# Kernel tuning notes

Measured on AMD Instinct MI355X. Metric: run time of the kernel, lower is better.

Reference implementation:

```python
import jax, jax.numpy as jnp
import numpy as np

WS = 8       # window size
HEADS = 2    # num_heads hardcoded in CFPT's Swin_transformer blocks


def _to_windows(t, ws):
    # t: [B, H, W, C] -> [B*nWin, ws*ws, C]
    B, H, W, C = t.shape
    t = t.reshape(B, H // ws, ws, W // ws, ws, C)
    t = t.transpose(0, 1, 3, 2, 4, 5)
    return t.reshape(-1, ws * ws, C)


def _from_windows(t, B, H, W, ws):
    # t: [B*nWin, ws*ws, C] -> [B, H, W, C]
    C = t.shape[-1]
    t = t.reshape(B, H // ws, W // ws, ws, ws, C)
    t = t.transpose(0, 1, 3, 2, 4, 5)
    return t.reshape(B, H, W, C)


def swin_cross_attn(x, y, Wq, Wk, Wv, Wo):
    # Windowed cross-attention: queries from x, keys/values from y.
    # x, y: [B, C, H, W]; Wq/Wk/Wv/Wo: [C, C] (bias-free, no position embedding).
    B, C, H, W = x.shape
    dh = C // HEADS
    xw = _to_windows(x.transpose(0, 2, 3, 1), WS)   # [Bn, T, C], T = WS*WS
    yw = _to_windows(y.transpose(0, 2, 3, 1), WS)
    q = jnp.einsum('btc,dc->btd', xw, Wq)
    k = jnp.einsum('btc,dc->btd', yw, Wk)
    v = jnp.einsum('btc,dc->btd', yw, Wv)
    Bn, T, _ = q.shape
    q = q.reshape(Bn, T, HEADS, dh)
    k = k.reshape(Bn, T, HEADS, dh)
    v = v.reshape(Bn, T, HEADS, dh)
    scale = jnp.asarray(dh, x.dtype) ** -0.5
    scores = jnp.einsum('bqhd,bkhd->bhqk', q, k) * scale   # [Bn, H, T, T]
    attn = jax.nn.softmax(scores, axis=-1)
    o = jnp.einsum('bhqk,bkhd->bqhd', attn, v).reshape(Bn, T, C)
    o = jnp.einsum('btc,dc->btd', o, Wo)
    return _from_windows(o, B, H, W, WS).transpose(0, 3, 1, 2)  # [B, C, H, W]


def setup_inputs() -> dict:
    key = jax.random.key(0)
    ks = jax.random.split(key, 6)
    C = 256
    shapes = [(4, C, 128, 128), (4, C, 64, 64), (4, C, 32, 32), (4, C, 16, 16)]
    feats = [jax.random.normal(ks[i], s, jnp.float32) for i, s in enumerate(shapes)]
    w1 = jax.random.normal(ks[4], (4, 4, C, C), jnp.float32) * 0.02
    w2 = jax.random.normal(ks[5], (4, 4, C, C), jnp.float32) * 0.02
    return {"feat0": feats[0], "feat1": feats[1], "feat2": feats[2],
            "feat3": feats[3], "w1": w1, "w2": w2}


def reference(feat0, feat1, feat2, feat3, w1, w2):
    feats = [feat0, feat1, feat2, feat3]
    l = feats[0].shape[0] // 2
    outs = []
    for i, f in enumerate(feats):
        f1, f2 = f[:l], f[l:]
        # sequential cross-update, as in the original loop body
        f1 = jax.nn.relu(f1 + swin_cross_attn(f1, f2, w1[i, 0], w1[i, 1], w1[i, 2], w1[i, 3]))
        f2 = jax.nn.relu(f2 + swin_cross_attn(f2, f1, w2[i, 0], w2[i, 1], w2[i, 2], w2[i, 3]))
        outs.append(jnp.concatenate([f1, f2], axis=0))
    return tuple(outs)
```

## Files before the change

### kernel.cpp

```cpp
#include <hip/hip_runtime.h>


using bf16x8 = __attribute__((ext_vector_type(8))) __bf16;
using f32x4  = __attribute__((ext_vector_type(4))) float;
using u16x4  = __attribute__((ext_vector_type(4))) unsigned short;
using u16x8  = __attribute__((ext_vector_type(8))) unsigned short;

__device__ __forceinline__ unsigned short f2bf(float f){
  unsigned int x = __float_as_uint(f);
  x += 0x7FFFu + ((x >> 16) & 1u);
  return (unsigned short)(x >> 16);
}
__device__ __forceinline__ float bf2f(unsigned short u){
  return __uint_as_float((unsigned int)u << 16);
}
__device__ __forceinline__ void store_bf4(unsigned short* dst, f32x4 v){
  u16x4 o;
  o[0]=f2bf(v[0]); o[1]=f2bf(v[1]); o[2]=f2bf(v[2]); o[3]=f2bf(v[3]);
  *reinterpret_cast<u16x4*>(dst) = o;
}

#define MFMA16 __builtin_amdgcn_mfma_f32_16x16x32_bf16

__global__ void wcvt_kernel(const float* __restrict__ w1,
                            const float* __restrict__ w2,
                            unsigned short* __restrict__ dst){
  int i = blockIdx.x * 256 + threadIdx.x;
  const float4* src = (i < 262144) ? (reinterpret_cast<const float4*>(w1) + i)
                                   : (reinterpret_cast<const float4*>(w2) + (i - 262144));
  float4 v = *src;
  u16x4 o; o[0]=f2bf(v.x); o[1]=f2bf(v.y); o[2]=f2bf(v.z); o[3]=f2bf(v.w);
  reinterpret_cast<u16x4*>(dst)[i] = o;
}

__global__ __launch_bounds__(256, 2) void xpose_kernel(
    const float* __restrict__ g0, const float* __restrict__ g1,
    const float* __restrict__ g2, const float* __restrict__ g3,
    unsigned short* __restrict__ Ft)
{
  __shared__ float T[64][65];
  int bid = blockIdx.x;
  int r; const float* feat; int Hl; size_t tbase;
  if (bid < 4096){ r = bid;        feat = g0; Hl = 128; tbase = 0; }
  else if (bid < 5120){ r = bid - 4096; feat = g1; Hl = 64;  tbase = 65536; }
  else if (bid < 5376){ r = bid - 5120; feat = g2; Hl = 32;  tbase = 81920; }
  else { r = bid - 5376; feat = g3; Hl = 16;  tbase = 86016; }
  size_t HW = (size_t)Hl * Hl;
  int hw64 = (int)(HW >> 6);
  int bat = r / (4 * hw64);
  int r2 = r - bat * 4 * hw64;
  int ct = r2 / hw64, hwt = r2 - ct * hw64;

  const float* src = feat + (size_t)bat * HW * 256 + (size_t)(ct * 64) * HW + (size_t)hwt * 64;
  int tid = threadIdx.x;
  int cq = tid >> 4, hw0 = (tid & 15) * 4;
  #pragma unroll
  for (int p = 0; p < 4; ++p){
    int c = p * 16 + cq;
    const float* sp = src + (size_t)c * HW + hw0;
    float4 v = *reinterpret_cast<const float4*>(sp);
    T[c][hw0] = v.x; T[c][hw0+1] = v.y; T[c][hw0+2] = v.z; T[c][hw0+3] = v.w;
  }
  __syncthreads();
  unsigned short* dst = Ft + (tbase + (size_t)bat * HW + (size_t)hwt * 64) * 256 + ct * 64;
  #pragma unroll
  for (int p = 0; p < 2; ++p){
    int id = p * 256 + tid;
    int t = id >> 3, c0 = (id & 7) * 8;
    u16x8 o;
    #pragma unroll
    for (int j = 0; j < 8; ++j) o[j] = f2bf(T[c0 + j][t]);
    *reinterpret_cast<u16x8*>(dst + (size_t)t * 256 + c0) = o;
  }
}

__global__ __launch_bounds__(256, 2) void untrans_kernel(
    const unsigned short* __restrict__ Gt, float* __restrict__ outb)
{
  __shared__ float T[64][65];
  int bid = blockIdx.x;
  int r; int Hl; size_t tbase, ooff;
  if (bid < 4096){ r = bid;        Hl = 128; tbase = 0;     ooff = 0; }
  else if (bid < 5120){ r = bid - 4096; Hl = 64; tbase = 65536; ooff = 16777216; }
  else if (bid < 5376){ r = bid - 5120; Hl = 32; tbase = 81920; ooff = 20971520; }
  else { r = bid - 5376; Hl = 16; tbase = 86016; ooff = 22020096; }
  size_t HW = (size_t)Hl * Hl;
  int hw64 = (int)(HW >> 6);
  int bat = r / (4 * hw64);
  int r2 = r - bat * 4 * hw64;
  int ct = r2 / hw64, hwt = r2 - ct * hw64;

  const unsigned short* src = Gt + (tbase + (size_t)bat * HW + (size_t)hwt * 64) * 256 + ct * 64;
  int tid = threadIdx.x;
  #pragma unroll
  for (int p = 0; p < 2; ++p){
    int id = p * 256 + tid;
    int t = id >> 3, c0 = (id & 7) * 8;
    u16x8 v = *reinterpret_cast<const u16x8*>(src + (size_t)t * 256 + c0);
    #pragma unroll
    for (int j = 0; j < 8; ++j) T[t][c0 + j] = bf2f(v[j]);
  }
  __syncthreads();
  float* dst = outb + ooff + (size_t)bat * HW * 256 + (size_t)(ct * 64) * HW + (size_t)hwt * 64;
  int cq = tid >> 4, hw0 = (tid & 15) * 4;
  #pragma unroll
  for (int p = 0; p < 4; ++p){
    int c = p * 16 + cq;
    float4 v;
    v.x = T[hw0][c]; v.y = T[hw0+1][c]; v.z = T[hw0+2][c]; v.w = T[hw0+3][c];
    *reinterpret_cast<float4*>(dst + (size_t)c * HW + hw0) = v;
  }
}

struct WinGeo { int H, W, b, lvl; size_t HW, winoff, tbase, ooff; };

__device__ __forceinline__ WinGeo decode_win(int win){
  WinGeo g; int wloc;
  if (win < 512){ g.lvl = 0; wloc = win;      g.H = 128; g.tbase = 0;     g.ooff = 0; }
  else if (win < 640){ g.lvl = 1; wloc = win - 512; g.H = 64; g.tbase = 65536; g.ooff = 16777216; }
  else if (win < 672){ g.lvl = 2; wloc = win - 640; g.H = 32; g.tbase = 81920; g.ooff = 20971520; }
  else { g.lvl = 3; wloc = win - 672; g.H = 16; g.tbase = 86016; g.ooff = 22020096; }
  g.W = g.H; g.HW = (size_t)g.H * g.W;
  int nww = g.H >> 3, npb = nww * nww;
  g.b = wloc / npb;
  int r = wloc - g.b * npb;
  int wh = r / nww, ww = r - wh * nww;
  g.winoff = (size_t)(wh * 8) * g.W + (size_t)(ww * 8);
  return g;
}

__global__ __launch_bounds__(256, 2) void swin_win(
    const unsigned short* __restrict__ Ft, const unsigned short* __restrict__ Gtin,
    const unsigned short* __restrict__ wball,
    unsigned short* __restrict__ Gt, int phase)
{
  __shared__ alignas(16) unsigned short A[64*264];
  __shared__ alignas(16) unsigned short B[256*72];
  int win = blockIdx.x;
  WinGeo g = decode_win(win);
  int tid = threadIdx.x;
  int w = tid >> 6, l = tid & 63, l15 = l & 15, l4 = l >> 4, wd = w * 64;
  int h = w >> 1, tc = w & 1;

  int batx = (phase == 0) ? g.b : g.b + 2;
  const unsigned short* Sx = Ft + (g.tbase + (size_t)batx * g.HW) * 256;
  const unsigned short* Sy = (phase == 0)
      ? Ft + (g.tbase + (size_t)(g.b + 2) * g.HW) * 256
      : Gtin + (g.tbase + (size_t)g.b * g.HW) * 256;
  unsigned short* Gout = Gt + (g.tbase + (size_t)batx * g.HW) * 256;

  size_t rowo[4];
  #pragma unroll
  for (int ni = 0; ni < 4; ++ni){
    int t = ni * 16 + l15;
    rowo[ni] = ((size_t)g.winoff + (size_t)(t >> 3) * g.W + (t & 7)) * 256;
  }
  const unsigned short* Wbase = wball + ((size_t)(phase * 16 + g.lvl * 4) << 16);
  const unsigned short* Wq = Wbase;
  const unsigned short* Wk = Wbase + 65536;
  const unsigned short* Wv = Wbase + 131072;
  const unsigned short* Wo = Wbase + 196608;

  f32x4 av[4][4];
  {
    f32x4 ak[4][4];
    #pragma unroll
    for (int i = 0; i < 4; ++i)
      #pragma unroll
      for (int j = 0; j < 4; ++j){ ak[i][j] = f32x4{0.f,0.f,0.f,0.f}; av[i][j] = f32x4{0.f,0.f,0.f,0.f}; }
    #pragma unroll
    for (int ks = 0; ks < 8; ++ks){
      int k0 = ks * 32 + l4 * 8;
      bf16x8 tf[4], kf[4], vf[4];
      #pragma unroll
      for (int i = 0; i < 4; ++i){
        tf[i] = *reinterpret_cast<const bf16x8*>(Sy + rowo[i] + k0);
        kf[i] = *reinterpret_cast<const bf16x8*>(Wk + (size_t)((wd + i*16 + l15) * 256 + k0));
        vf[i] = *reinterpret_cast<const bf16x8*>(Wv + (size_t)((wd + i*16 + l15) * 256 + k0));
      }
      __builtin_amdgcn_s_setprio(1);
      #pragma unroll
      for (int mi = 0; mi < 4; ++mi)
        #pragma unroll
        for (int ni = 0; ni < 4; ++ni){
          ak[mi][ni] = MFMA16(kf[mi], tf[ni], ak[mi][ni], 0, 0, 0);
          av[mi][ni] = MFMA16(tf[mi], vf[ni], av[mi][ni], 0, 0, 0);
        }
      __builtin_amdgcn_s_setprio(0);
    }
    #pragma unroll
    for (int mi = 0; mi < 4; ++mi){
      int d0 = wd + mi*16 + l4*4;
      #pragma unroll
      for (int ni = 0; ni < 4; ++ni)
        store_bf4(&A[(ni*16 + l15) * 264 + d0], ak[mi][ni]);
    }
  }

  {
    f32x4 aq[4][4];
    #pragma unroll
    for (int i = 0; i < 4; ++i)
      #pragma unroll
      for (int j = 0; j < 4; ++j) aq[i][j] = f32x4{0.f,0.f,0.f,0.f};
    #pragma unroll
    for (int ks = 0; ks < 8; ++ks){
      int k0 = ks * 32 + l4 * 8;
      bf16x8 tf[4], wf[4];
      #pragma unroll
      for (int i = 0; i < 4; ++i){
        tf[i] = *reinterpret_cast<const bf16x8*>(Sx + rowo[i] + k0);
        wf[i] = *reinterpret_cast<const bf16x8*>(Wq + (size_t)((wd + i*16 + l15) * 256 + k0));
      }
      __builtin_amdgcn_s_setprio(1);
      #pragma unroll
      for (int mi = 0; mi < 4; ++mi)
        #pragma unroll
        for (int ni = 0; ni < 4; ++ni)
          aq[mi][ni] = MFMA16(wf[mi], tf[ni], aq[mi][ni], 0, 0, 0);
      __builtin_amdgcn_s_setprio(0);
    }
    #pragma unroll
    for (int mi = 0; mi < 4; ++mi){
      int d0 = wd + mi*16 + l4*4;
      #pragma unroll
      for (int ni = 0; ni < 4; ++ni)
        store_bf4(&B[(ni*16 + l15) * 264 + d0], aq[mi][ni]);
    }
  }
  __syncthreads();

  f32x4 s[4][2];
  #pragma unroll
  for (int i = 0; i < 4; ++i){ s[i][0] = f32x4{0.f,0.f,0.f,0.f}; s[i][1] = f32x4{0.f,0.f,0.f,0.f}; }
  #pragma unroll
  for (int ks = 0; ks < 4; ++ks){
    int k0 = h * 128 + ks * 32 + l4 * 8;
    bf16x8 a[4], bb[2];
    #pragma unroll
    for (int mi = 0; mi < 4; ++mi)
      a[mi] = *reinterpret_cast<const bf16x8*>(&A[(mi*16 + l15) * 264 + k0]);
    #pragma unroll
    for (int ni = 0; ni < 2; ++ni)
      bb[ni] = *reinterpret_cast<const bf16x8*>(&B[(tc*32 + ni*16 + l15) * 264 + k0]);
    __builtin_amdgcn_s_setprio(1);
    #pragma unroll
    for (int mi = 0; mi < 4; ++mi)
      #pragma unroll
      for (int ni = 0; ni < 2; ++ni)
        s[mi][ni] = MFMA16(a[mi], bb[ni], s[mi][ni], 0, 0, 0);
    __builtin_amdgcn_s_setprio(0);
  }
  __syncthreads();

  #pragma unroll
  for (int mi = 0; mi < 4; ++mi){
    int u0 = mi*16 + l4*4;
    #pragma unroll
    for (int ni = 0; ni < 4; ++ni)
      store_bf4(&B[(wd + ni*16 + l15) * 72 + u0], av[mi][ni]);
  }

  const float SCL = 0.08838834764831845f;
  #pragma unroll
  for (int ni = 0; ni < 2; ++ni){
    float m = s[0][ni][0];
    #pragma unroll
    for (int mi = 0; mi < 4; ++mi)
      #pragma unroll
      for (int reg = 0; reg < 4; ++reg) m = fmaxf(m, s[mi][ni][reg]);
    m = fmaxf(m, __shfl_xor(m, 16));
    m = fmaxf(m, __shfl_xor(m, 32));
    float sum = 0.f;
    #pragma unroll
    for (int mi = 0; mi < 4; ++mi)
      #pragma unroll
      for (int reg = 0; reg < 4; ++reg){
        float e = __expf((s[mi][ni][reg] - m) * SCL);
        s[mi][ni][reg] = e; sum += e;
      }
    sum += __shfl_xor(sum, 16);
    sum += __shfl_xor(sum, 32);
    float rs = 1.0f / sum;
    int t = tc*32 + ni*16 + l15;
    #pragma unroll
    for (int mi = 0; mi < 4; ++mi){
      f32x4 pv;
      #pragma unroll
      for (int reg = 0; reg < 4; ++reg) pv[reg] = s[mi][ni][reg] * rs;
      store_bf4(&A[h * 4608 + t * 72 + mi*16 + l4*4], pv);
    }
  }
  __syncthreads();

  f32x4 acc[4][4];
  #pragma unroll
  for (int i = 0; i < 4; ++i)
    #pragma unroll
    for (int j = 0; j < 4; ++j) acc[i][j] = f32x4{0.f,0.f,0.f,0.f};
  #pragma unroll
  for (int ks = 0; ks < 2; ++ks){
    int k0 = ks * 32 + l4 * 8;
    bf16x8 a[4], bb[4];
    #pragma unroll
    for (int mi = 0; mi < 4; ++mi)
      a[mi] = *reinterpret_cast<const bf16x8*>(&B[(wd + mi*16 + l15) * 72 + k0]);
    #pragma unroll
    for (int ni = 0; ni < 4; ++ni)
      bb[ni] = *reinterpret_cast<const bf16x8*>(&A[h * 4608 + (ni*16 + l15) * 72 + k0]);
    __builtin_amdgcn_s_setprio(1);
    #pragma unroll
    for (int mi = 0; mi < 4; ++mi)
      #pragma unroll
      for (int ni = 0; ni < 4; ++ni)
        acc[mi][ni] = MFMA16(a[mi], bb[ni], acc[mi][ni], 0, 0, 0);
    __builtin_amdgcn_s_setprio(0);
  }
  __syncthreads();
  #pragma unroll
  for (int mi = 0; mi < 4; ++mi){
    int c0 = wd + mi*16 + l4*4;
    #pragma unroll
    for (int ni = 0; ni < 4; ++ni)
      store_bf4(&A[(ni*16 + l15) * 264 + c0], acc[mi][ni]);
  }
  __syncthreads();

  #pragma unroll
  for (int i = 0; i < 4; ++i)
    #pragma unroll
    for (int j = 0; j < 4; ++j) acc[i][j] = f32x4{0.f,0.f,0.f,0.f};
  #pragma unroll
  for (int ks = 0; ks < 8; ++ks){
    int k0 = ks * 32 + l4 * 8;
    bf16x8 a[4], bb[4];
    #pragma unroll
    for (int mi = 0; mi < 4; ++mi)
      a[mi] = *reinterpret_cast<const bf16x8*>(Wo + (size_t)((wd + mi*16 + l15) * 256 + k0));
    #pragma unroll
    for (int ni = 0; ni < 4; ++ni)
      bb[ni] = *reinterpret_cast<const bf16x8*>(&A[(ni*16 + l15) * 264 + k0]);
    __builtin_amdgcn_s_setprio(1);
    #pragma unroll
    for (int mi = 0; mi < 4; ++mi)
      #pragma unroll
      for (int ni = 0; ni < 4; ++ni)
        acc[mi][ni] = MFMA16(a[mi], bb[ni], acc[mi][ni], 0, 0, 0);
    __builtin_amdgcn_s_setprio(0);
  }
  __syncthreads();
  #pragma unroll
  for (int mi = 0; mi < 4; ++mi){
    int c0 = wd + mi*16 + l4*4;
    #pragma unroll
    for (int ni = 0; ni < 4; ++ni)
      store_bf4(&A[(ni*16 + l15) * 264 + c0], acc[mi][ni]);
  }
  __syncthreads();

  #pragma unroll
  for (int p = 0; p < 8; ++p){
    int id = p * 256 + tid;
    int t = id >> 5, c = (id & 31) * 8;
    size_t ro = ((size_t)g.winoff + (size_t)(t >> 3) * g.W + (t & 7)) * 256 + c;
    u16x8 ov = *reinterpret_cast<const u16x8*>(&A[t * 264 + c]);
    u16x8 rv = *reinterpret_cast<const u16x8*>(Sx + ro);
    u16x8 o;
    #pragma unroll
    for (int j = 0; j < 8; ++j)
      o[j] = f2bf(fmaxf(bf2f(ov[j]) + bf2f(rv[j]), 0.f));
    *reinterpret_cast<u16x8*>(Gout + ro) = o;
  }
}

__global__ __launch_bounds__(256, 1) void swin_phase(
    const float* __restrict__ g0, const float* __restrict__ g1,
    const float* __restrict__ g2, const float* __restrict__ g3,
    const unsigned short* __restrict__ wball,
    float* __restrict__ outb, int phase)
{
  __shared__ alignas(16) unsigned short R0[64*264];
  __shared__ alignas(16) unsigned short R1[64*264];
  __shared__ alignas(16) unsigned short R2[256*72];
  __shared__ alignas(16) unsigned short R3[64*264];

  int bid = blockIdx.x;
  WinGeo g = decode_win(bid);
  const float* feat = (g.lvl == 0) ? g0 : (g.lvl == 1) ? g1 : (g.lvl == 2) ? g2 : g3;
  size_t CHW = g.HW * 256;

  const float* xsrc; const float* ysrc; float* outp;
  if (phase == 0){
    xsrc = feat + (size_t)g.b * CHW + g.winoff;
    ysrc = feat + (size_t)(g.b + 2) * CHW + g.winoff;
    outp = outb + g.ooff + (size_t)g.b * CHW + g.winoff;
  } else {
    xsrc = feat + (size_t)(g.b + 2) * CHW + g.winoff;
    ysrc = outb + g.ooff + (size_t)g.b * CHW + g.winoff;
    outp = outb + g.ooff + (size_t)(g.b + 2) * CHW + g.winoff;
  }
  const unsigned short* Wq = wball + ((size_t)(phase * 16 + g.lvl * 4) << 16);
  const unsigned short* Wk = Wq + 65536;
  const unsigned short* Wv = Wq + 2 * 65536;
  const unsigned short* Wo = Wq + 3 * 65536;

  int tid = threadIdx.x;
  int w = tid >> 6, l = tid & 63, l15 = l & 15, l4 = l >> 4, wd = w * 64;
  int hi0 = l >> 3, wi0 = l & 7;

  {
    const float* p0 = ysrc + (size_t)hi0 * g.W + wi0;
    #pragma unroll
    for (int oc = 0; oc < 8; ++oc){
      int c0 = (oc * 4 + w) * 8;
      const float* p = p0 + (size_t)c0 * g.HW;
      u16x8 uv;
      #pragma unroll
      for (int j = 0; j < 8; ++j) uv[j] = f2bf(p[(size_t)j * g.HW]);
      *reinterpret_cast<u16x8*>(&R0[l * 264 + c0]) = uv;
    }
  }
  __syncthreads();
  {
    f32x4 acc[4][4];
    #pragma unroll
    for (int i = 0; i < 4; ++i)
      #pragma unroll
      for (int j = 0; j < 4; ++j) acc[i][j] = f32x4{0.f,0.f,0.f,0.f};
    #pragma unroll
    for (int ks = 0; ks < 8; ++ks){
      int k0 = ks * 32 + l4 * 8;
      bf16x8 a[4], bb[4];
      #pragma unroll
      for (int mi = 0; mi < 4; ++mi)
        a[mi] = *reinterpret_cast<const bf16x8*>(Wk + (size_t)((wd + mi*16 + l15) * 256 + k0));
      #pragma unroll
      for (int ni = 0; ni < 4; ++ni)
        bb[ni] = *reinterpret_cast<const bf16x8*>(&R0[(ni*16 + l15) * 264 + k0]);
      #pragma unroll
      for (int mi = 0; mi < 4; ++mi)
        #pragma unroll
        for (int ni = 0; ni < 4; ++ni)
          acc[mi][ni] = MFMA16(a[mi], bb[ni], acc[mi][ni], 0, 0, 0);
    }
    #pragma unroll
    for (int mi = 0; mi < 4; ++mi){
      int d0 = wd + mi*16 + l4*4;
      #pragma unroll
      for (int ni = 0; ni < 4; ++ni)
        store_bf4(&R1[(ni*16 + l15) * 264 + d0], acc[mi][ni]);
    }
  }
  {
    f32x4 acc[4][4];
    #pragma unroll
    for (int i = 0; i < 4; ++i)
      #pragma unroll
      for (int j = 0; j < 4; ++j) acc[i][j] = f32x4{0.f,0.f,0.f,0.f};
    #pragma unroll
    for (int ks = 0; ks < 8; ++ks){
      int k0 = ks * 32 + l4 * 8;
      bf16x8 a[4], bb[4];
      #pragma unroll
      for (int mi = 0; mi < 4; ++mi)
        a[mi] = *reinterpret_cast<const bf16x8*>(&R0[(mi*16 + l15) * 264 + k0]);
      #pragma unroll
      for (int ni = 0; ni < 4; ++ni)
        bb[ni] = *reinterpret_cast<const bf16x8*>(Wv + (size_t)((wd + ni*16 + l15) * 256 + k0));
      #pragma unroll
      for (int mi = 0; mi < 4; ++mi)
        #pragma unroll
        for (int ni = 0; ni < 4; ++ni)
          acc[mi][ni] = MFMA16(a[mi], bb[ni], acc[mi][ni], 0, 0, 0);
    }
    #pragma unroll
    for (int mi = 0; mi < 4; ++mi){
      int u0 = mi*16 + l4*4;
      #pragma unroll
      for (int ni = 0; ni < 4; ++ni)
        store_bf4(&R2[(wd + ni*16 + l15) * 72 + u0], acc[mi][ni]);
    }
  }
  __syncthreads();
  {
    const float* p0 = xsrc + (size_t)hi0 * g.W + wi0;
    #pragma unroll
    for (int oc = 0; oc < 8; ++oc){
      int c0 = (oc * 4 + w) * 8;
      const float* p = p0 + (size_t)c0 * g.HW;
      u16x8 uv;
      #pragma unroll
      for (int j = 0; j < 8; ++j) uv[j] = f2bf(p[(size_t)j * g.HW]);
      *reinterpret_cast<u16x8*>(&R0[l * 264 + c0]) = uv;
    }
  }
  __syncthreads();
  {
    f32x4 acc[4][4];
    #pragma unroll
    for (int i = 0; i < 4; ++i)
      #pragma unroll
      for (int j = 0; j < 4; ++j) acc[i][j] = f32x4{0.f,0.f,0.f,0.f};
    #pragma unroll
    for (int ks = 0; ks < 8; ++ks){
      int k0 = ks * 32 + l4 * 8;
      bf16x8 a[4], bb[4];
      #pragma unroll
      for (int mi = 0; mi < 4; ++mi)
        a[mi] = *reinterpret_cast<const bf16x8*>(Wq + (size_t)((wd + mi*16 + l15) * 256 + k0));
      #pragma unroll
      for (int ni = 0; ni < 4; ++ni)
        bb[ni] = *reinterpret_cast<const bf16x8*>(&R0[(ni*16 + l15) * 264 + k0]);
      #pragma unroll
      for (int mi = 0; mi < 4; ++mi)
        #pragma unroll
        for (int ni = 0; ni < 4; ++ni)
          acc[mi][ni] = MFMA16(a[mi], bb[ni], acc[mi][ni], 0, 0, 0);
    }
    #pragma unroll
    for (int mi = 0; mi < 4; ++mi){
      int d0 = wd + mi*16 + l4*4;
      #pragma unroll
      for (int ni = 0; ni < 4; ++ni)
        store_bf4(&R3[(ni*16 + l15) * 264 + d0], acc[mi][ni]);
    }
  }
  __syncthreads();

  int h = w >> 1, tc = w & 1;
  {
    f32x4 s[4][2];
    #pragma unroll
    for (int i = 0; i < 4; ++i){ s[i][0] = f32x4{0.f,0.f,0.f,0.f}; s[i][1] = f32x4{0.f,0.f,0.f,0.f}; }
    #pragma unroll
    for (int ks = 0; ks < 4; ++ks){
      int k0 = h * 128 + ks * 32 + l4 * 8;
      bf16x8 a[4], bb[2];
      #pragma unroll
      for (int mi = 0; mi < 4; ++mi)
        a[mi] = *reinterpret_cast<const bf16x8*>(&R1[(mi*16 + l15) * 264 + k0]);
      #pragma unroll
      for (int ni = 0; ni < 2; ++ni)
        bb[ni] = *reinterpret_cast<const bf16x8*>(&R3[(tc*32 + ni*16 + l15) * 264 + k0]);
      #pragma unroll
      for (int mi = 0; mi < 4; ++mi)
        #pragma unroll
        for (int ni = 0; ni < 2; ++ni)
          s[mi][ni] = MFMA16(a[mi], bb[ni], s[mi][ni], 0, 0, 0);
    }
    __syncthreads();
    const float SCL = 0.08838834764831845f;
    unsigned short* P = R1;
    #pragma unroll
    for (int ni = 0; ni < 2; ++ni){
      float m = s[0][ni][0];
      #pragma unroll
      for (int mi = 0; mi < 4; ++mi)
        #pragma unroll
        for (int reg = 0; reg < 4; ++reg) m = fmaxf(m, s[mi][ni][reg]);
      m = fmaxf(m, __shfl_xor(m, 16));
      m = fmaxf(m, __shfl_xor(m, 32));
      float sum = 0.f;
      #pragma unroll
      for (int mi = 0; mi < 4; ++mi)
        #pragma unroll
        for (int reg = 0; reg < 4; ++reg){
          float e = __expf((s[mi][ni][reg] - m) * SCL);
          s[mi][ni][reg] = e; sum += e;
        }
      sum += __shfl_xor(sum, 16);
      sum += __shfl_xor(sum, 32);
      float rs = 1.0f / sum;
      int t = tc*32 + ni*16 + l15;
      #pragma unroll
      for (int mi = 0; mi < 4; ++mi){
        f32x4 pv;
        #pragma unroll
        for (int reg = 0; reg < 4; ++reg) pv[reg] = s[mi][ni][reg] * rs;
        store_bf4(&P[h * 4608 + t * 72 + mi*16 + l4*4], pv);
      }
    }
  }
  __syncthreads();
  {
    int wdh = h * 128 + tc * 64;
    f32x4 acc[4][4];
    #pragma unroll
    for (int i = 0; i < 4; ++i)
      #pragma unroll
      for (int j = 0; j < 4; ++j) acc[i][j] = f32x4{0.f,0.f,0.f,0.f};
    const unsigned short* P = R1;
    #pragma unroll
    for (int ks = 0; ks < 2; ++ks){
      int k0 = ks * 32 + l4 * 8;
      bf16x8 a[4], bb[4];
      #pragma unroll
      for (int mi = 0; mi < 4; ++mi)
        a[mi] = *reinterpret_cast<const bf16x8*>(&R2[(wdh + mi*16 + l15) * 72 + k0]);
      #pragma unroll
      for (int ni = 0; ni < 4; ++ni)
        bb[ni] = *reinterpret_cast<const bf16x8*>(&P[h * 4608 + (ni*16 + l15) * 72 + k0]);
      #pragma unroll
      for (int mi = 0; mi < 4; ++mi)
        #pragma unroll
        for (int ni = 0; ni < 4; ++ni)
          acc[mi][ni] = MFMA16(a[mi], bb[ni], acc[mi][ni], 0, 0, 0);
    }
    #pragma unroll
    for (int mi = 0; mi < 4; ++mi){
      int c0 = wdh + mi*16 + l4*4;
      #pragma unroll
      for (int ni = 0; ni < 4; ++ni)
        store_bf4(&R0[(ni*16 + l15) * 264 + c0], acc[mi][ni]);
    }
  }
  __syncthreads();
  {
    f32x4 acc[4][4];
    #pragma unroll
    for (int i = 0; i < 4; ++i)
      #pragma unroll
      for (int j = 0; j < 4; ++j) acc[i][j] = f32x4{0.f,0.f,0.f,0.f};
    #pragma unroll
    for (int ks = 0; ks < 8; ++ks){
      int k0 = ks * 32 + l4 * 8;
      bf16x8 a[4], bb[4];
      #pragma unroll
      for (int mi = 0; mi < 4; ++mi)
        a[mi] = *reinterpret_cast<const bf16x8*>(Wo + (size_t)((wd + mi*16 + l15) * 256 + k0));
      #pragma unroll
      for (int ni = 0; ni < 4; ++ni)
        bb[ni] = *reinterpret_cast<const bf16x8*>(&R0[(ni*16 + l15) * 264 + k0]);
      #pragma unroll
      for (int mi = 0; mi < 4; ++mi)
        #pragma unroll
        for (int ni = 0; ni < 4; ++ni)
          acc[mi][ni] = MFMA16(a[mi], bb[ni], acc[mi][ni], 0, 0, 0);
    }
    #pragma unroll
    for (int mi = 0; mi < 4; ++mi){
      #pragma unroll
      for (int ni = 0; ni < 4; ++ni){
        int t = ni*16 + l15, thi = t >> 3, twi = t & 7;
        size_t base = (size_t)(wd + mi*16 + l4*4) * g.HW + (size_t)thi * g.W + twi;
        #pragma unroll
        for (int reg = 0; reg < 4; ++reg){
          float res = xsrc[base + (size_t)reg * g.HW];
          float v = acc[mi][ni][reg] + res;
          outp[base + (size_t)reg * g.HW] = fmaxf(v, 0.f);
        }
      }
    }
  }
}

extern "C" void kernel_launch(void* const* d_in, const int* in_sizes, int n_in,
                              void* d_out, int out_size, void* d_ws, size_t ws_size,
                              hipStream_t stream) {
  (void)in_sizes; (void)n_in; (void)out_size;
  const float* f0 = (const float*)d_in[0];
  const float* f1 = (const float*)d_in[1];
  const float* f2 = (const float*)d_in[2];
  const float* f3 = (const float*)d_in[3];
  const float* w1 = (const float*)d_in[4];
  const float* w2 = (const float*)d_in[5];
  float* out = (float*)d_out;

  unsigned short* wbf = (unsigned short*)d_ws;
  const size_t WBF_B = 4194304;
  const size_t FT_B  = 44564480;
  const size_t need  = WBF_B + 2 * FT_B;

  wcvt_kernel<<<2048, 256, 0, stream>>>(w1, w2, wbf);

  if (ws_size >= need){
    char* base = (char*)d_ws + WBF_B;
    unsigned short* Ft = (unsigned short*)(base);
    unsigned short* Gt = (unsigned short*)(base + FT_B);

    xpose_kernel<<<5440, 256, 0, stream>>>(f0, f1, f2, f3, Ft);
    for (int phase = 0; phase < 2; ++phase)
      swin_win<<<680, 256, 0, stream>>>(Ft, Gt, wbf, Gt, phase);
    untrans_kernel<<<5440, 256, 0, stream>>>(Gt, out);
  } else {
    swin_phase<<<680, 256, 0, stream>>>(f0, f1, f2, f3, wbf, out, 0);
    swin_phase<<<680, 256, 0, stream>>>(f0, f1, f2, f3, wbf, out, 1);
  }
}
```

Measured before the change: 198.9 us.

## Fuse both cross-attention phases per window and rebalance windows across blocks

The two per-phase launches are merged into one kernel that, per window, computes the f1 update, keeps the updated f1 tile in shared memory, and feeds it straight into the f2 update's key/value projection. This avoids a second launch and the round trip of the phase-0 result through global memory. The grid shrinks to 512 blocks, and every third block in the first 504 also takes one extra small-level window, so the 680 windows are spread unevenly. Each block now does twice the serial work, which lengthens the critical path and lowers parallelism on a GPU with many CUs.

```diff
diff --git a/kernel.cpp b/kernel.cpp
--- a/kernel.cpp
+++ b/kernel.cpp
@@ -129,247 +129,461 @@
   return g;
 }
 
-__global__ __launch_bounds__(256, 2) void swin_win(
-    const unsigned short* __restrict__ Ft, const unsigned short* __restrict__ Gtin,
+__global__ __launch_bounds__(256, 2) void swin_fused(
+    const unsigned short* __restrict__ Ft,
     const unsigned short* __restrict__ wball,
-    unsigned short* __restrict__ Gt, int phase)
+    unsigned short* __restrict__ Gt)
 {
   __shared__ alignas(16) unsigned short A[64*264];
   __shared__ alignas(16) unsigned short B[256*72];
-  int win = blockIdx.x;
-  WinGeo g = decode_win(win);
+  int bid = blockIdx.x;
   int tid = threadIdx.x;
   int w = tid >> 6, l = tid & 63, l15 = l & 15, l4 = l >> 4, wd = w * 64;
   int h = w >> 1, tc = w & 1;
-
-  int batx = (phase == 0) ? g.b : g.b + 2;
-  const unsigned short* Sx = Ft + (g.tbase + (size_t)batx * g.HW) * 256;
-  const unsigned short* Sy = (phase == 0)
-      ? Ft + (g.tbase + (size_t)(g.b + 2) * g.HW) * 256
-      : Gtin + (g.tbase + (size_t)g.b * g.HW) * 256;
-  unsigned short* Gout = Gt + (g.tbase + (size_t)batx * g.HW) * 256;
-
-  size_t rowo[4];
-  #pragma unroll
-  for (int ni = 0; ni < 4; ++ni){
-    int t = ni * 16 + l15;
-    rowo[ni] = ((size_t)g.winoff + (size_t)(t >> 3) * g.W + (t & 7)) * 256;
-  }
-  const unsigned short* Wbase = wball + ((size_t)(phase * 16 + g.lvl * 4) << 16);
-  const unsigned short* Wq = Wbase;
-  const unsigned short* Wk = Wbase + 65536;
-  const unsigned short* Wv = Wbase + 131072;
-  const unsigned short* Wo = Wbase + 196608;
-
-  f32x4 av[4][4];
-  {
-    f32x4 ak[4][4];
-    #pragma unroll
-    for (int i = 0; i < 4; ++i)
-      #pragma unroll
-      for (int j = 0; j < 4; ++j){ ak[i][j] = f32x4{0.f,0.f,0.f,0.f}; av[i][j] = f32x4{0.f,0.f,0.f,0.f}; }
-    #pragma unroll
-    for (int ks = 0; ks < 8; ++ks){
-      int k0 = ks * 32 + l4 * 8;
-      bf16x8 tf[4], kf[4], vf[4];
-      #pragma unroll
-      for (int i = 0; i < 4; ++i){
-        tf[i] = *reinterpret_cast<const bf16x8*>(Sy + rowo[i] + k0);
-        kf[i] = *reinterpret_cast<const bf16x8*>(Wk + (size_t)((wd + i*16 + l15) * 256 + k0));
-        vf[i] = *reinterpret_cast<const bf16x8*>(Wv + (size_t)((wd + i*16 + l15) * 256 + k0));
-      }
-      __builtin_amdgcn_s_setprio(1);
-      #pragma unroll
-      for (int mi = 0; mi < 4; ++mi)
-        #pragma unroll
-        for (int ni = 0; ni < 4; ++ni){
-          ak[mi][ni] = MFMA16(kf[mi], tf[ni], ak[mi][ni], 0, 0, 0);
-          av[mi][ni] = MFMA16(tf[mi], vf[ni], av[mi][ni], 0, 0, 0);
-        }
-      __builtin_amdgcn_s_setprio(0);
-    }
-    #pragma unroll
-    for (int mi = 0; mi < 4; ++mi){
-      int d0 = wd + mi*16 + l4*4;
-      #pragma unroll
-      for (int ni = 0; ni < 4; ++ni)
-        store_bf4(&A[(ni*16 + l15) * 264 + d0], ak[mi][ni]);
-    }
-  }
-
-  {
-    f32x4 aq[4][4];
-    #pragma unroll
-    for (int i = 0; i < 4; ++i)
-      #pragma unroll
-      for (int j = 0; j < 4; ++j) aq[i][j] = f32x4{0.f,0.f,0.f,0.f};
-    #pragma unroll
-    for (int ks = 0; ks < 8; ++ks){
-      int k0 = ks * 32 + l4 * 8;
-      bf16x8 tf[4], wf[4];
-      #pragma unroll
-      for (int i = 0; i < 4; ++i){
-        tf[i] = *reinterpret_cast<const bf16x8*>(Sx + rowo[i] + k0);
-        wf[i] = *reinterpret_cast<const bf16x8*>(Wq + (size_t)((wd + i*16 + l15) * 256 + k0));
-      }
-      __builtin_amdgcn_s_setprio(1);
-      #pragma unroll
-      for (int mi = 0; mi < 4; ++mi)
-        #pragma unroll
-        for (int ni = 0; ni < 4; ++ni)
-          aq[mi][ni] = MFMA16(wf[mi], tf[ni], aq[mi][ni], 0, 0, 0);
-      __builtin_amdgcn_s_setprio(0);
-    }
-    #pragma unroll
-    for (int mi = 0; mi < 4; ++mi){
-      int d0 = wd + mi*16 + l4*4;
-      #pragma unroll
-      for (int ni = 0; ni < 4; ++ni)
-        store_bf4(&B[(ni*16 + l15) * 264 + d0], aq[mi][ni]);
-    }
-  }
-  __syncthreads();
-
-  f32x4 s[4][2];
-  #pragma unroll
-  for (int i = 0; i < 4; ++i){ s[i][0] = f32x4{0.f,0.f,0.f,0.f}; s[i][1] = f32x4{0.f,0.f,0.f,0.f}; }
-  #pragma unroll
-  for (int ks = 0; ks < 4; ++ks){
-    int k0 = h * 128 + ks * 32 + l4 * 8;
-    bf16x8 a[4], bb[2];
-    #pragma unroll
-    for (int mi = 0; mi < 4; ++mi)
-      a[mi] = *reinterpret_cast<const bf16x8*>(&A[(mi*16 + l15) * 264 + k0]);
-    #pragma unroll
-    for (int ni = 0; ni < 2; ++ni)
-      bb[ni] = *reinterpret_cast<const bf16x8*>(&B[(tc*32 + ni*16 + l15) * 264 + k0]);
-    __builtin_amdgcn_s_setprio(1);
-    #pragma unroll
-    for (int mi = 0; mi < 4; ++mi)
-      #pragma unroll
-      for (int ni = 0; ni < 2; ++ni)
-        s[mi][ni] = MFMA16(a[mi], bb[ni], s[mi][ni], 0, 0, 0);
-    __builtin_amdgcn_s_setprio(0);
-  }
-  __syncthreads();
-
-  #pragma unroll
-  for (int mi = 0; mi < 4; ++mi){
-    int u0 = mi*16 + l4*4;
-    #pragma unroll
-    for (int ni = 0; ni < 4; ++ni)
-      store_bf4(&B[(wd + ni*16 + l15) * 72 + u0], av[mi][ni]);
-  }
-
   const float SCL = 0.08838834764831845f;
-  #pragma unroll
-  for (int ni = 0; ni < 2; ++ni){
-    float m = s[0][ni][0];
-    #pragma unroll
-    for (int mi = 0; mi < 4; ++mi)
-      #pragma unroll
-      for (int reg = 0; reg < 4; ++reg) m = fmaxf(m, s[mi][ni][reg]);
-    m = fmaxf(m, __shfl_xor(m, 16));
-    m = fmaxf(m, __shfl_xor(m, 32));
-    float sum = 0.f;
-    #pragma unroll
-    for (int mi = 0; mi < 4; ++mi)
-      #pragma unroll
-      for (int reg = 0; reg < 4; ++reg){
-        float e = __expf((s[mi][ni][reg] - m) * SCL);
-        s[mi][ni][reg] = e; sum += e;
-      }
-    sum += __shfl_xor(sum, 16);
-    sum += __shfl_xor(sum, 32);
-    float rs = 1.0f / sum;
-    int t = tc*32 + ni*16 + l15;
-    #pragma unroll
-    for (int mi = 0; mi < 4; ++mi){
-      f32x4 pv;
-      #pragma unroll
-      for (int reg = 0; reg < 4; ++reg) pv[reg] = s[mi][ni][reg] * rs;
-      store_bf4(&A[h * 4608 + t * 72 + mi*16 + l4*4], pv);
-    }
-  }
-  __syncthreads();
-
-  f32x4 acc[4][4];
-  #pragma unroll
-  for (int i = 0; i < 4; ++i)
-    #pragma unroll
-    for (int j = 0; j < 4; ++j) acc[i][j] = f32x4{0.f,0.f,0.f,0.f};
-  #pragma unroll
-  for (int ks = 0; ks < 2; ++ks){
-    int k0 = ks * 32 + l4 * 8;
-    bf16x8 a[4], bb[4];
-    #pragma unroll
-    for (int mi = 0; mi < 4; ++mi)
-      a[mi] = *reinterpret_cast<const bf16x8*>(&B[(wd + mi*16 + l15) * 72 + k0]);
-    #pragma unroll
-    for (int ni = 0; ni < 4; ++ni)
-      bb[ni] = *reinterpret_cast<const bf16x8*>(&A[h * 4608 + (ni*16 + l15) * 72 + k0]);
-    __builtin_amdgcn_s_setprio(1);
-    #pragma unroll
-    for (int mi = 0; mi < 4; ++mi)
-      #pragma unroll
-      for (int ni = 0; ni < 4; ++ni)
-        acc[mi][ni] = MFMA16(a[mi], bb[ni], acc[mi][ni], 0, 0, 0);
-    __builtin_amdgcn_s_setprio(0);
-  }
-  __syncthreads();
-  #pragma unroll
-  for (int mi = 0; mi < 4; ++mi){
-    int c0 = wd + mi*16 + l4*4;
-    #pragma unroll
-    for (int ni = 0; ni < 4; ++ni)
-      store_bf4(&A[(ni*16 + l15) * 264 + c0], acc[mi][ni]);
-  }
-  __syncthreads();
-
-  #pragma unroll
-  for (int i = 0; i < 4; ++i)
-    #pragma unroll
-    for (int j = 0; j < 4; ++j) acc[i][j] = f32x4{0.f,0.f,0.f,0.f};
-  #pragma unroll
-  for (int ks = 0; ks < 8; ++ks){
-    int k0 = ks * 32 + l4 * 8;
-    bf16x8 a[4], bb[4];
-    #pragma unroll
-    for (int mi = 0; mi < 4; ++mi)
-      a[mi] = *reinterpret_cast<const bf16x8*>(Wo + (size_t)((wd + mi*16 + l15) * 256 + k0));
-    #pragma unroll
-    for (int ni = 0; ni < 4; ++ni)
-      bb[ni] = *reinterpret_cast<const bf16x8*>(&A[(ni*16 + l15) * 264 + k0]);
-    __builtin_amdgcn_s_setprio(1);
-    #pragma unroll
-    for (int mi = 0; mi < 4; ++mi)
-      #pragma unroll
-      for (int ni = 0; ni < 4; ++ni)
-        acc[mi][ni] = MFMA16(a[mi], bb[ni], acc[mi][ni], 0, 0, 0);
-    __builtin_amdgcn_s_setprio(0);
-  }
-  __syncthreads();
-  #pragma unroll
-  for (int mi = 0; mi < 4; ++mi){
-    int c0 = wd + mi*16 + l4*4;
-    #pragma unroll
-    for (int ni = 0; ni < 4; ++ni)
-      store_bf4(&A[(ni*16 + l15) * 264 + c0], acc[mi][ni]);
-  }
-  __syncthreads();
-
-  #pragma unroll
-  for (int p = 0; p < 8; ++p){
-    int id = p * 256 + tid;
-    int t = id >> 5, c = (id & 31) * 8;
-    size_t ro = ((size_t)g.winoff + (size_t)(t >> 3) * g.W + (t & 7)) * 256 + c;
-    u16x8 ov = *reinterpret_cast<const u16x8*>(&A[t * 264 + c]);
-    u16x8 rv = *reinterpret_cast<const u16x8*>(Sx + ro);
-    u16x8 o;
-    #pragma unroll
-    for (int j = 0; j < 8; ++j)
-      o[j] = f2bf(fmaxf(bf2f(ov[j]) + bf2f(rv[j]), 0.f));
-    *reinterpret_cast<u16x8*>(Gout + ro) = o;
+
+  int nwin = ((bid % 3) == 0 && bid < 504) ? 2 : 1;
+  for (int wi = 0; wi < nwin; ++wi){
+    if (wi) __syncthreads();
+    int win = wi ? (512 + bid / 3) : bid;
+    WinGeo g = decode_win(win);
+    const unsigned short* Sx = Ft + (g.tbase + (size_t)g.b * g.HW) * 256;
+    const unsigned short* Sy = Ft + (g.tbase + (size_t)(g.b + 2) * g.HW) * 256;
+    unsigned short* GoutA = Gt + (g.tbase + (size_t)g.b * g.HW) * 256;
+    unsigned short* GoutB = Gt + (g.tbase + (size_t)(g.b + 2) * g.HW) * 256;
+
+    size_t rowo[4];
+    #pragma unroll
+    for (int ni = 0; ni < 4; ++ni){
+      int t = ni * 16 + l15;
+      rowo[ni] = ((size_t)g.winoff + (size_t)(t >> 3) * g.W + (t & 7)) * 256;
+    }
+    const unsigned short* W1 = wball + ((size_t)(g.lvl * 4) << 16);
+    const unsigned short* W2 = wball + ((size_t)(16 + g.lvl * 4) << 16);
+
+    {
+      f32x4 av[4][4];
+      {
+        f32x4 ak[4][4];
+        #pragma unroll
+        for (int i = 0; i < 4; ++i)
+          #pragma unroll
+          for (int j = 0; j < 4; ++j){ ak[i][j] = f32x4{0.f,0.f,0.f,0.f}; av[i][j] = f32x4{0.f,0.f,0.f,0.f}; }
+        #pragma unroll
+        for (int ks = 0; ks < 8; ++ks){
+          int k0 = ks * 32 + l4 * 8;
+          bf16x8 tf[4], kf[4], vf[4];
+          #pragma unroll
+          for (int i = 0; i < 4; ++i){
+            tf[i] = *reinterpret_cast<const bf16x8*>(Sy + rowo[i] + k0);
+            kf[i] = *reinterpret_cast<const bf16x8*>(W1 + 65536 + (size_t)((wd + i*16 + l15) * 256 + k0));
+            vf[i] = *reinterpret_cast<const bf16x8*>(W1 + 131072 + (size_t)((wd + i*16 + l15) * 256 + k0));
+          }
+          __builtin_amdgcn_s_setprio(1);
+          #pragma unroll
+          for (int mi = 0; mi < 4; ++mi)
+            #pragma unroll
+            for (int ni = 0; ni < 4; ++ni){
+              ak[mi][ni] = MFMA16(kf[mi], tf[ni], ak[mi][ni], 0, 0, 0);
+              av[mi][ni] = MFMA16(tf[mi], vf[ni], av[mi][ni], 0, 0, 0);
+            }
+          __builtin_amdgcn_s_setprio(0);
+        }
+        #pragma unroll
+        for (int mi = 0; mi < 4; ++mi){
+          int d0 = wd + mi*16 + l4*4;
+          #pragma unroll
+          for (int ni = 0; ni < 4; ++ni)
+            store_bf4(&A[(ni*16 + l15) * 264 + d0], ak[mi][ni]);
+        }
+      }
+      {
+        f32x4 aq[4][4];
+        #pragma unroll
+        for (int i = 0; i < 4; ++i)
+          #pragma unroll
+          for (int j = 0; j < 4; ++j) aq[i][j] = f32x4{0.f,0.f,0.f,0.f};
+        #pragma unroll
+        for (int ks = 0; ks < 8; ++ks){
+          int k0 = ks * 32 + l4 * 8;
+          bf16x8 tf[4], wf[4];
+          #pragma unroll
+          for (int i = 0; i < 4; ++i){
+            tf[i] = *reinterpret_cast<const bf16x8*>(Sx + rowo[i] + k0);
+            wf[i] = *reinterpret_cast<const bf16x8*>(W1 + (size_t)((wd + i*16 + l15) * 256 + k0));
+          }
+          __builtin_amdgcn_s_setprio(1);
+          #pragma unroll
+          for (int mi = 0; mi < 4; ++mi)
+            #pragma unroll
+            for (int ni = 0; ni < 4; ++ni)
+              aq[mi][ni] = MFMA16(wf[mi], tf[ni], aq[mi][ni], 0, 0, 0);
+          __builtin_amdgcn_s_setprio(0);
+        }
+        #pragma unroll
+        for (int mi = 0; mi < 4; ++mi){
+          int d0 = wd + mi*16 + l4*4;
+          #pragma unroll
+          for (int ni = 0; ni < 4; ++ni)
+            store_bf4(&B[(ni*16 + l15) * 264 + d0], aq[mi][ni]);
+        }
+      }
+      __syncthreads();
+
+      f32x4 s[4][2];
+      #pragma unroll
+      for (int i = 0; i < 4; ++i){ s[i][0] = f32x4{0.f,0.f,0.f,0.f}; s[i][1] = f32x4{0.f,0.f,0.f,0.f}; }
+      #pragma unroll
+      for (int ks = 0; ks < 4; ++ks){
+        int k0 = h * 128 + ks * 32 + l4 * 8;
+        bf16x8 a[4], bb[2];
+        #pragma unroll
+        for (int mi = 0; mi < 4; ++mi)
+          a[mi] = *reinterpret_cast<const bf16x8*>(&A[(mi*16 + l15) * 264 + k0]);
+        #pragma unroll
+        for (int ni = 0; ni < 2; ++ni)
+          bb[ni] = *reinterpret_cast<const bf16x8*>(&B[(tc*32 + ni*16 + l15) * 264 + k0]);
+        __builtin_amdgcn_s_setprio(1);
+        #pragma unroll
+        for (int mi = 0; mi < 4; ++mi)
+          #pragma unroll
+          for (int ni = 0; ni < 2; ++ni)
+            s[mi][ni] = MFMA16(a[mi], bb[ni], s[mi][ni], 0, 0, 0);
+        __builtin_amdgcn_s_setprio(0);
+      }
+      __syncthreads();
+
+      #pragma unroll
+      for (int mi = 0; mi < 4; ++mi){
+        int u0 = mi*16 + l4*4;
+        #pragma unroll
+        for (int ni = 0; ni < 4; ++ni)
+          store_bf4(&B[(wd + ni*16 + l15) * 72 + u0], av[mi][ni]);
+      }
+      #pragma unroll
+      for (int ni = 0; ni < 2; ++ni){
+        float m = s[0][ni][0];
+        #pragma unroll
+        for (int mi = 0; mi < 4; ++mi)
+          #pragma unroll
+          for (int reg = 0; reg < 4; ++reg) m = fmaxf(m, s[mi][ni][reg]);
+        m = fmaxf(m, __shfl_xor(m, 16));
+        m = fmaxf(m, __shfl_xor(m, 32));
+        float sum = 0.f;
+        #pragma unroll
+        for (int mi = 0; mi < 4; ++mi)
+          #pragma unroll
+          for (int reg = 0; reg < 4; ++reg){
+            float e = __expf((s[mi][ni][reg] - m) * SCL);
+            s[mi][ni][reg] = e; sum += e;
+          }
+        sum += __shfl_xor(sum, 16);
+        sum += __shfl_xor(sum, 32);
+        float rs = 1.0f / sum;
+        int t = tc*32 + ni*16 + l15;
+        #pragma unroll
+        for (int mi = 0; mi < 4; ++mi){
+          f32x4 pv;
+          #pragma unroll
+          for (int reg = 0; reg < 4; ++reg) pv[reg] = s[mi][ni][reg] * rs;
+          store_bf4(&A[h * 4608 + t * 72 + mi*16 + l4*4], pv);
+        }
+      }
+      __syncthreads();
+
+      f32x4 acc[4][4];
+      #pragma unroll
+      for (int i = 0; i < 4; ++i)
+        #pragma unroll
+        for (int j = 0; j < 4; ++j) acc[i][j] = f32x4{0.f,0.f,0.f,0.f};
+      #pragma unroll
+      for (int ks = 0; ks < 2; ++ks){
+        int k0 = ks * 32 + l4 * 8;
+        bf16x8 a[4], bb[4];
+        #pragma unroll
+        for (int mi = 0; mi < 4; ++mi)
+          a[mi] = *reinterpret_cast<const bf16x8*>(&B[(wd + mi*16 + l15) * 72 + k0]);
+        #pragma unroll
+        for (int ni = 0; ni < 4; ++ni)
+          bb[ni] = *reinterpret_cast<const bf16x8*>(&A[h * 4608 + (ni*16 + l15) * 72 + k0]);
+        __builtin_amdgcn_s_setprio(1);
+        #pragma unroll
+        for (int mi = 0; mi < 4; ++mi)
+          #pragma unroll
+          for (int ni = 0; ni < 4; ++ni)
+            acc[mi][ni] = MFMA16(a[mi], bb[ni], acc[mi][ni], 0, 0, 0);
+        __builtin_amdgcn_s_setprio(0);
+      }
+      __syncthreads();
+      #pragma unroll
+      for (int mi = 0; mi < 4; ++mi){
+        int c0 = wd + mi*16 + l4*4;
+        #pragma unroll
+        for (int ni = 0; ni < 4; ++ni)
+          store_bf4(&A[(ni*16 + l15) * 264 + c0], acc[mi][ni]);
+      }
+      __syncthreads();
+
+      #pragma unroll
+      for (int i = 0; i < 4; ++i)
+        #pragma unroll
+        for (int j = 0; j < 4; ++j) acc[i][j] = f32x4{0.f,0.f,0.f,0.f};
+      #pragma unroll
+      for (int ks = 0; ks < 8; ++ks){
+        int k0 = ks * 32 + l4 * 8;
+        bf16x8 a[4], bb[4];
+        #pragma unroll
+        for (int mi = 0; mi < 4; ++mi)
+          a[mi] = *reinterpret_cast<const bf16x8*>(W1 + 196608 + (size_t)((wd + mi*16 + l15) * 256 + k0));
+        #pragma unroll
+        for (int ni = 0; ni < 4; ++ni)
+          bb[ni] = *reinterpret_cast<const bf16x8*>(&A[(ni*16 + l15) * 264 + k0]);
+        __builtin_amdgcn_s_setprio(1);
+        #pragma unroll
+        for (int mi = 0; mi < 4; ++mi)
+          #pragma unroll
+          for (int ni = 0; ni < 4; ++ni)
+            acc[mi][ni] = MFMA16(a[mi], bb[ni], acc[mi][ni], 0, 0, 0);
+        __builtin_amdgcn_s_setprio(0);
+      }
+      __syncthreads();
+      #pragma unroll
+      for (int mi = 0; mi < 4; ++mi){
+        int c0 = wd + mi*16 + l4*4;
+        #pragma unroll
+        for (int ni = 0; ni < 4; ++ni)
+          store_bf4(&A[(ni*16 + l15) * 264 + c0], acc[mi][ni]);
+      }
+      __syncthreads();
+
+      #pragma unroll
+      for (int p = 0; p < 8; ++p){
+        int id = p * 256 + tid;
+        int t = id >> 5, c = (id & 31) * 8;
+        size_t ro = ((size_t)g.winoff + (size_t)(t >> 3) * g.W + (t & 7)) * 256 + c;
+        u16x8 ov = *reinterpret_cast<const u16x8*>(&A[t * 264 + c]);
+        u16x8 rv = *reinterpret_cast<const u16x8*>(Sx + ro);
+        u16x8 o;
+        #pragma unroll
+        for (int j = 0; j < 8; ++j)
+          o[j] = f2bf(fmaxf(bf2f(ov[j]) + bf2f(rv[j]), 0.f));
+        *reinterpret_cast<u16x8*>(GoutA + ro) = o;
+        *reinterpret_cast<u16x8*>(&A[t * 264 + c]) = o;
+      }
+      __syncthreads();
+    }
+
+    {
+      f32x4 av[4][4];
+      {
+        f32x4 ak[4][4];
+        #pragma unroll
+        for (int i = 0; i < 4; ++i)
+          #pragma unroll
+          for (int j = 0; j < 4; ++j){ ak[i][j] = f32x4{0.f,0.f,0.f,0.f}; av[i][j] = f32x4{0.f,0.f,0.f,0.f}; }
+        #pragma unroll
+        for (int ks = 0; ks < 8; ++ks){
+          int k0 = ks * 32 + l4 * 8;
+          bf16x8 tf[4], kf[4], vf[4];
+          #pragma unroll
+          for (int i = 0; i < 4; ++i){
+            tf[i] = *reinterpret_cast<const bf16x8*>(&A[(i*16 + l15) * 264 + k0]);
+            kf[i] = *reinterpret_cast<const bf16x8*>(W2 + 65536 + (size_t)((wd + i*16 + l15) * 256 + k0));
+            vf[i] = *reinterpret_cast<const bf16x8*>(W2 + 131072 + (size_t)((wd + i*16 + l15) * 256 + k0));
+          }
+          __builtin_amdgcn_s_setprio(1);
+          #pragma unroll
+          for (int mi = 0; mi < 4; ++mi)
+            #pragma unroll
+            for (int ni = 0; ni < 4; ++ni){
+              ak[mi][ni] = MFMA16(kf[mi], tf[ni], ak[mi][ni], 0, 0, 0);
+              av[mi][ni] = MFMA16(tf[mi], vf[ni], av[mi][ni], 0, 0, 0);
+            }
+          __builtin_amdgcn_s_setprio(0);
+        }
+        #pragma unroll
+        for (int mi = 0; mi < 4; ++mi){
+          int d0 = wd + mi*16 + l4*4;
+          #pragma unroll
+          for (int ni = 0; ni < 4; ++ni)
+            store_bf4(&B[(ni*16 + l15) * 264 + d0], ak[mi][ni]);
+        }
+      }
+      __syncthreads();
+
+      {
+        f32x4 aq[4][4];
+        #pragma unroll
+        for (int i = 0; i < 4; ++i)
+          #pragma unroll
+          for (int j = 0; j < 4; ++j) aq[i][j] = f32x4{0.f,0.f,0.f,0.f};
+        #pragma unroll
+        for (int ks = 0; ks < 8; ++ks){
+          int k0 = ks * 32 + l4 * 8;
+          bf16x8 tf[4], wf[4];
+          #pragma unroll
+          for (int i = 0; i < 4; ++i){
+            tf[i] = *reinterpret_cast<const bf16x8*>(Sy + rowo[i] + k0);
+            wf[i] = *reinterpret_cast<const bf16x8*>(W2 + (size_t)((wd + i*16 + l15) * 256 + k0));
+          }
+          __builtin_amdgcn_s_setprio(1);
+          #pragma unroll
+          for (int mi = 0; mi < 4; ++mi)
+            #pragma unroll
+            for (int ni = 0; ni < 4; ++ni)
+              aq[mi][ni] = MFMA16(wf[mi], tf[ni], aq[mi][ni], 0, 0, 0);
+          __builtin_amdgcn_s_setprio(0);
+        }
+        #pragma unroll
+        for (int mi = 0; mi < 4; ++mi){
+          int d0 = wd + mi*16 + l4*4;
+          #pragma unroll
+          for (int ni = 0; ni < 4; ++ni)
+            store_bf4(&A[(ni*16 + l15) * 264 + d0], aq[mi][ni]);
+        }
+      }
+      __syncthreads();
+
+      f32x4 s[4][2];
+      #pragma unroll
+      for (int i = 0; i < 4; ++i){ s[i][0] = f32x4{0.f,0.f,0.f,0.f}; s[i][1] = f32x4{0.f,0.f,0.f,0.f}; }
+      #pragma unroll
+      for (int ks = 0; ks < 4; ++ks){
+        int k0 = h * 128 + ks * 32 + l4 * 8;
+        bf16x8 a[4], bb[2];
+        #pragma unroll
+        for (int mi = 0; mi < 4; ++mi)
+          a[mi] = *reinterpret_cast<const bf16x8*>(&B[(mi*16 + l15) * 264 + k0]);
+        #pragma unroll
+        for (int ni = 0; ni < 2; ++ni)
+          bb[ni] = *reinterpret_cast<const bf16x8*>(&A[(tc*32 + ni*16 + l15) * 264 + k0]);
+        __builtin_amdgcn_s_setprio(1);
+        #pragma unroll
+        for (int mi = 0; mi < 4; ++mi)
+          #pragma unroll
+          for (int ni = 0; ni < 2; ++ni)
+            s[mi][ni] = MFMA16(a[mi], bb[ni], s[mi][ni], 0, 0, 0);
+        __builtin_amdgcn_s_setprio(0);
+      }
+      __syncthreads();
+
+      #pragma unroll
+      for (int mi = 0; mi < 4; ++mi){
+        int u0 = mi*16 + l4*4;
+        #pragma unroll
+        for (int ni = 0; ni < 4; ++ni)
+          store_bf4(&B[(wd + ni*16 + l15) * 72 + u0], av[mi][ni]);
+      }
+      #pragma unroll
+      for (int ni = 0; ni < 2; ++ni){
+        float m = s[0][ni][0];
+        #pragma unroll
+        for (int mi = 0; mi < 4; ++mi)
+          #pragma unroll
+          for (int reg = 0; reg < 4; ++reg) m = fmaxf(m, s[mi][ni][reg]);
+        m = fmaxf(m, __shfl_xor(m, 16));
+        m = fmaxf(m, __shfl_xor(m, 32));
+        float sum = 0.f;
+        #pragma unroll
+        for (int mi = 0; mi < 4; ++mi)
+          #pragma unroll
+          for (int reg = 0; reg < 4; ++reg){
+            float e = __expf((s[mi][ni][reg] - m) * SCL);
+            s[mi][ni][reg] = e; sum += e;
+          }
+        sum += __shfl_xor(sum, 16);
+        sum += __shfl_xor(sum, 32);
+        float rs = 1.0f / sum;
+        int t = tc*32 + ni*16 + l15;
+        #pragma unroll
+        for (int mi = 0; mi < 4; ++mi){
+          f32x4 pv;
+          #pragma unroll
+          for (int reg = 0; reg < 4; ++reg) pv[reg] = s[mi][ni][reg] * rs;
+          store_bf4(&A[h * 4608 + t * 72 + mi*16 + l4*4], pv);
+        }
+      }
+      __syncthreads();
+
+      f32x4 acc[4][4];
+      #pragma unroll
+      for (int i = 0; i < 4; ++i)
+        #pragma unroll
+        for (int j = 0; j < 4; ++j) acc[i][j] = f32x4{0.f,0.f,0.f,0.f};
+      #pragma unroll
+      for (int ks = 0; ks < 2; ++ks){
+        int k0 = ks * 32 + l4 * 8;
+        bf16x8 a[4], bb[4];
+        #pragma unroll
+        for (int mi = 0; mi < 4; ++mi)
+          a[mi] = *reinterpret_cast<const bf16x8*>(&B[(wd + mi*16 + l15) * 72 + k0]);
+        #pragma unroll
+        for (int ni = 0; ni < 4; ++ni)
+          bb[ni] = *reinterpret_cast<const bf16x8*>(&A[h * 4608 + (ni*16 + l15) * 72 + k0]);
+        __builtin_amdgcn_s_setprio(1);
+        #pragma unroll
+        for (int mi = 0; mi < 4; ++mi)
+          #pragma unroll
+          for (int ni = 0; ni < 4; ++ni)
+            acc[mi][ni] = MFMA16(a[mi], bb[ni], acc[mi][ni], 0, 0, 0);
+        __builtin_amdgcn_s_setprio(0);
+      }
+      __syncthreads();
+      #pragma unroll
+      for (int mi = 0; mi < 4; ++mi){
+        int c0 = wd + mi*16 + l4*4;
+        #pragma unroll
+        for (int ni = 0; ni < 4; ++ni)
+          store_bf4(&A[(ni*16 + l15) * 264 + c0], acc[mi][ni]);
+      }
+      __syncthreads();
+
+      #pragma unroll
+      for (int i = 0; i < 4; ++i)
+        #pragma unroll
+        for (int j = 0; j < 4; ++j) acc[i][j] = f32x4{0.f,0.f,0.f,0.f};
+      #pragma unroll
+      for (int ks = 0; ks < 8; ++ks){
+        int k0 = ks * 32 + l4 * 8;
+        bf16x8 a[4], bb[4];
+        #pragma unroll
+        for (int mi = 0; mi < 4; ++mi)
+          a[mi] = *reinterpret_cast<const bf16x8*>(W2 + 196608 + (size_t)((wd + mi*16 + l15) * 256 + k0));
+        #pragma unroll
+        for (int ni = 0; ni < 4; ++ni)
+          bb[ni] = *reinterpret_cast<const bf16x8*>(&A[(ni*16 + l15) * 264 + k0]);
+        __builtin_amdgcn_s_setprio(1);
+        #pragma unroll
+        for (int mi = 0; mi < 4; ++mi)
+          #pragma unroll
+          for (int ni = 0; ni < 4; ++ni)
+            acc[mi][ni] = MFMA16(a[mi], bb[ni], acc[mi][ni], 0, 0, 0);
+        __builtin_amdgcn_s_setprio(0);
+      }
+      __syncthreads();
+      #pragma unroll
+      for (int mi = 0; mi < 4; ++mi){
+        int c0 = wd + mi*16 + l4*4;
+        #pragma unroll
+        for (int ni = 0; ni < 4; ++ni)
+          store_bf4(&A[(ni*16 + l15) * 264 + c0], acc[mi][ni]);
+      }
+      __syncthreads();
+
+      #pragma unroll
+      for (int p = 0; p < 8; ++p){
+        int id = p * 256 + tid;
+        int t = id >> 5, c = (id & 31) * 8;
+        size_t ro = ((size_t)g.winoff + (size_t)(t >> 3) * g.W + (t & 7)) * 256 + c;
+        u16x8 ov = *reinterpret_cast<const u16x8*>(&A[t * 264 + c]);
+        u16x8 rv = *reinterpret_cast<const u16x8*>(Sy + ro);
+        u16x8 o;
+        #pragma unroll
+        for (int j = 0; j < 8; ++j)
+          o[j] = f2bf(fmaxf(bf2f(ov[j]) + bf2f(rv[j]), 0.f));
+        *reinterpret_cast<u16x8*>(GoutB + ro) = o;
+      }
+    }
   }
 }
 
@@ -679,8 +893,7 @@
     unsigned short* Gt = (unsigned short*)(base + FT_B);
 
     xpose_kernel<<<5440, 256, 0, stream>>>(f0, f1, f2, f3, Ft);
-    for (int phase = 0; phase < 2; ++phase)
-      swin_win<<<680, 256, 0, stream>>>(Ft, Gt, wbf, Gt, phase);
+    swin_fused<<<512, 256, 0, stream>>>(Ft, wbf, Gt);
     untrans_kernel<<<5440, 256, 0, stream>>>(Gt, out);
   } else {
     swin_phase<<<680, 256, 0, stream>>>(f0, f1, f2, f3, wbf, out, 0);
```

Result: slower. 220.5 us (+10.9%).
